# Optimization experiments

Hardware: AMD Instinct MI355X
Metric: run time of the kernel (lower is better)

## Reference

```python
import jax, jax.numpy as jnp
import numpy as np

TOP_K = 2

def setup_inputs() -> dict:
    key = jax.random.key(0)
    k1, k2, k3, k4, k5 = jax.random.split(key, 5)
    B, S, D, E, H = 1, 2048, 2048, 8, 5632
    scale = 0.02
    return {
        "x": jax.random.normal(k1, (B, S, D), dtype=jnp.float32),
        "gate_w": jax.random.normal(k2, (E, D), dtype=jnp.float32) * scale,
        "w1": jax.random.normal(k3, (E, H, D), dtype=jnp.float32) * scale,
        "w2": jax.random.normal(k4, (E, D, H), dtype=jnp.float32) * scale,
        "w3": jax.random.normal(k5, (E, H, D), dtype=jnp.float32) * scale,
    }


def reference(x, gate_w, w1, w2, w3):
    # x: [B, S, D]; gate_w: [E, D]; w1/w3: [E, H, D]; w2: [E, D, H]
    B, S, D = x.shape
    E = gate_w.shape[0]
    xf = x.reshape(-1, D)                      # [T, D]
    T = xf.shape[0]

    # Gate (gate_softmax=False): topk on raw scores, softmax over the top-k
    scores = xf @ gate_w.T                     # [T, E]
    expert_weights, expert_indices = jax.lax.top_k(scores, TOP_K)
    expert_weights = jax.nn.softmax(expert_weights, axis=-1)  # [T, K]

    # Scatter top-k weights to a dense [T, E] combine matrix (zeros elsewhere)
    combine = jnp.zeros((T, E), dtype=xf.dtype).at[
        jnp.arange(T)[:, None], expert_indices
    ].add(expert_weights)

    # SwiGLU FFN per expert, batched over the (small, fixed) expert axis.
    # Math identical to masked dispatch since combine is zero off the top-k.
    h = jax.nn.silu(jnp.einsum("td,ehd->eth", xf, w1)) \
        * jnp.einsum("td,ehd->eth", xf, w3)    # [E, T, H]
    ye = jnp.einsum("eth,edh->etd", h, w2)     # [E, T, D]

    # Weighted combine of top-k expert outputs per token
    y = jnp.einsum("etd,te->td", ye, combine)  # [T, D]
    return y.reshape(B, S, D)
```

## Files before the change

### kernel.cpp

```cpp
#include <hip/hip_runtime.h>
#include <hip/hip_bf16.h>

#define T_TOK 2048
#define DIM   2048
#define NE    8
#define NH    5632

typedef __attribute__((ext_vector_type(4))) float f32x4;
typedef __attribute__((ext_vector_type(8))) short short8;
typedef __attribute__((ext_vector_type(4))) unsigned int u32x4;
typedef __attribute__((ext_vector_type(4))) float float4v;

__device__ inline unsigned short f2bf(float f) {
    unsigned u = __builtin_bit_cast(unsigned, f);
    u += 0x7fffu + ((u >> 16) & 1u);
    return (unsigned short)(u >> 16);
}

__device__ __forceinline__ short8 pack8(float4v a, float4v b) {
    short8 o;
    o[0]=(short)f2bf(a[0]); o[1]=(short)f2bf(a[1]); o[2]=(short)f2bf(a[2]); o[3]=(short)f2bf(a[3]);
    o[4]=(short)f2bf(b[0]); o[5]=(short)f2bf(b[1]); o[6]=(short)f2bf(b[2]); o[7]=(short)f2bf(b[3]);
    return o;
}

__device__ __forceinline__ short8 cvt8(f32x4 lo, f32x4 hi) {
    u32x4 L = __builtin_bit_cast(u32x4, lo);
    u32x4 H = __builtin_bit_cast(u32x4, hi);
    u32x4 r;
    r[0] = __builtin_amdgcn_perm(L[1], L[0], 0x07060302u);
    r[1] = __builtin_amdgcn_perm(L[3], L[2], 0x07060302u);
    r[2] = __builtin_amdgcn_perm(H[1], H[0], 0x07060302u);
    r[3] = __builtin_amdgcn_perm(H[3], H[2], 0x07060302u);
    return __builtin_bit_cast(short8, r);
}

__device__ __forceinline__ void glds16(const void* g, void* l) {
    __builtin_amdgcn_global_load_lds((const __attribute__((address_space(1))) void*)g,
                                     (__attribute__((address_space(3))) void*)l, 16, 0, 0);
}

__global__ void k_cvt(const float* __restrict__ src, unsigned short* __restrict__ dst, int n8) {
    int i = blockIdx.x * blockDim.x + threadIdx.x;
    if (i >= n8) return;
    const float4v* xv = (const float4v*)src;
    ((short8*)dst)[i] = pack8(xv[2 * i], xv[2 * i + 1]);
}

__global__ void k_gate(const float* __restrict__ x, const float* __restrict__ gw,
                       int* __restrict__ rt_e, float* __restrict__ rt_w, int* __restrict__ cnt) {
    int wid = threadIdx.x >> 6, lane = threadIdx.x & 63;
    int t = blockIdx.x * 4 + wid;
    if (t >= T_TOK) return;
    float acc[NE];
#pragma unroll
    for (int e = 0; e < NE; e++) acc[e] = 0.f;
    const float* xr = x + (size_t)t * DIM;
    for (int d = lane; d < DIM; d += 64) {
        float xv = xr[d];
#pragma unroll
        for (int e = 0; e < NE; e++) acc[e] += xv * gw[e * DIM + d];
    }
#pragma unroll
    for (int e = 0; e < NE; e++) {
        float v = acc[e];
#pragma unroll
        for (int off = 32; off; off >>= 1) v += __shfl_xor(v, off);
        acc[e] = v;
    }
    if (lane == 0) {
        int i0 = 0; float s0 = acc[0];
#pragma unroll
        for (int e = 1; e < NE; e++) if (acc[e] > s0) { s0 = acc[e]; i0 = e; }
        int i1 = -1; float s1 = -1e30f;
#pragma unroll
        for (int e = 0; e < NE; e++) if (e != i0 && acc[e] > s1) { s1 = acc[e]; i1 = e; }
        float w0 = 1.f / (1.f + expf(s1 - s0));
        rt_e[2 * t] = i0; rt_e[2 * t + 1] = i1;
        rt_w[2 * t] = w0; rt_w[2 * t + 1] = 1.f - w0;
        atomicAdd(&cnt[i0], 1);
        atomicAdd(&cnt[i1], 1);
    }
}

__global__ void k_base(const int* __restrict__ cnt, int* __restrict__ base, int* __restrict__ pb) {
    if (threadIdx.x == 0) {
        int s = 0, p = 0;
        for (int e = 0; e < NE; e++) {
            base[e] = s; pb[e] = p;
            s += cnt[e];
            p += ((cnt[e] + 127) >> 7) << 7;
        }
    }
}

__global__ void k_assign(const int* __restrict__ rt_e, const float* __restrict__ rt_w,
                         const int* __restrict__ base, int* __restrict__ run,
                         int* __restrict__ tok, float* __restrict__ tw,
                         int* __restrict__ slotof) {
    int t = blockIdx.x * blockDim.x + threadIdx.x;
    if (t >= T_TOK) return;
#pragma unroll
    for (int k = 0; k < 2; k++) {
        int e = rt_e[2 * t + k];
        int p = atomicAdd(&run[e], 1);
        int g = base[e] + p;
        tok[g] = t;
        tw[g] = rt_w[2 * t + k];
        slotof[2 * t + k] = g;
    }
}

__global__ void k_xpack(const float* __restrict__ x,
                        const int* __restrict__ cnt, const int* __restrict__ base,
                        const int* __restrict__ pb, const int* __restrict__ tok,
                        unsigned short* __restrict__ xp) {
    int e = blockIdx.z, mt = blockIdx.y, kt = blockIdx.x;
    int c = cnt[e], m0 = mt * 128;
    if (m0 >= c) return;
    int gb = base[e];
    int ptile = (pb[e] >> 7) + mt;
    int lane = threadIdx.x & 63, w = threadIdx.x >> 6;
    int kc = lane & 7;
    unsigned short* db = xp + (size_t)ptile * 262144 + (size_t)kt * 8192;
#pragma unroll
    for (int it = 0; it < 4; ++it) {
        int rloc = it * 32 + w * 8 + (lane >> 3);
        int slot = m0 + rloc;
        int t = tok[gb + (slot < c ? slot : 0)];
        const float* s = x + (size_t)t * DIM + kt * 64 + kc * 8;
        *(short8*)(db + kc * 1024 + rloc * 8) = pack8(*(const float4v*)s, *(const float4v*)(s + 4));
    }
}

__global__ void k_combine(const float* __restrict__ ye, const int* __restrict__ slotof,
                          float* __restrict__ y) {
    int t = blockIdx.x;
    int s0 = slotof[2 * t], s1 = slotof[2 * t + 1];
    const float4v* a = (const float4v*)(ye + (size_t)s0 * DIM);
    const float4v* b = (const float4v*)(ye + (size_t)s1 * DIM);
    float4v* o = (float4v*)(y + (size_t)t * DIM);
    for (int i = threadIdx.x; i < DIM / 4; i += 256) {
        float4v va = a[i], vb = b[i];
        float4v r;
        r[0] = va[0] + vb[0]; r[1] = va[1] + vb[1];
        r[2] = va[2] + vb[2]; r[3] = va[3] + vb[3];
        o[i] = r;
    }
}

__launch_bounds__(256, 3)
__global__ void k_ffn1p(const unsigned short* __restrict__ xp,
                        const float* __restrict__ w1, const float* __restrict__ w3,
                        const int* __restrict__ cnt, const int* __restrict__ pb,
                        unsigned short* __restrict__ hb, int nwg,
                        const float* __restrict__ w2, unsigned short* __restrict__ w2p) {
    int bid = blockIdx.x;
    if (bid >= nwg) {
        int pid = bid - nwg;
        int kt = pid % 88;
        int r  = pid / 88;
        int nt = r & 15;
        int e  = r >> 4;
        int lane = threadIdx.x & 63, w = threadIdx.x >> 6;
        int kc = lane & 7;
        const float* sb = w2 + (size_t)e * DIM * NH;
        unsigned short* db = w2p + ((size_t)(e * 16 + nt) * 88 + kt) * 8192;
#pragma unroll
        for (int it = 0; it < 4; ++it) {
            int rloc = it * 32 + w * 8 + (lane >> 3);
            const float* s = sb + (size_t)(nt * 128 + rloc) * NH + kt * 64 + kc * 8;
            *(short8*)(db + kc * 1024 + rloc * 8) = pack8(*(const float4v*)s, *(const float4v*)(s + 4));
        }
        return;
    }

    int swz = (bid & 7) * (nwg >> 3) + (bid >> 3);
    int mt = swz & 15;
    int r2 = swz >> 4;
    int nt = r2 % 88;
    int e  = r2 / 88;
    int c  = cnt[e];
    int m0 = mt * 128;
    if (m0 >= c) return;
    int ptile = (pb[e] >> 7) + mt;

    __shared__ unsigned short As[8192];
    __shared__ float B1f[4096];
    __shared__ float B3f[4096];

    int tid = threadIdx.x;
    int lane = tid & 63, w = tid >> 6;
    int wm = w >> 1, wn = w & 1;
    int half = w & 1, wh = w >> 1;
    int p15 = lane & 15, rl0 = lane >> 4;

    const unsigned short* aB = xp + (size_t)ptile * 262144 + half * 512 + lane * 8;
    const float* w1e = w1 + (size_t)(e * NH + nt * 64) * DIM;
    const float* w3e = w3 + (size_t)(e * NH + nt * 64) * DIM;

    f32x4 acc1[4][2], acc3[4][2];
#pragma unroll
    for (int i = 0; i < 4; i++)
#pragma unroll
        for (int j = 0; j < 2; j++) { acc1[i][j] = (f32x4)0.f; acc3[i][j] = (f32x4)0.f; }

    for (int kt = 0; kt < 32; ++kt) {
        __syncthreads();
#pragma unroll
        for (int i = 0; i < 4; i++) {
            int kc = i * 2 + wh;
            glds16(aB + kt * 8192 + kc * 1024, (char*)As + kc * 2048 + half * 1024);
        }
#pragma unroll
        for (int i = 0; i < 4; i++) {
            int rloc = w * 16 + i * 4 + rl0;
            int q    = p15 ^ ((i * 4 + rl0) & 15);
            glds16(w1e + (size_t)rloc * DIM + kt * 64 + q * 4, (char*)B1f + (w * 16 + i * 4) * 256);
            glds16(w3e + (size_t)rloc * DIM + kt * 64 + q * 4, (char*)B3f + (w * 16 + i * 4) * 256);
        }
        asm volatile("s_waitcnt vmcnt(0)" ::: "memory");
        __syncthreads();
#pragma unroll
        for (int kh = 0; kh < 2; kh++) {
            int kc = kh * 4 + rl0;
            short8 a[4], b1[2], b3[2];
#pragma unroll
            for (int mf = 0; mf < 4; mf++) {
                int r = wm * 64 + mf * 16 + p15;
                a[mf] = *(const short8*)(As + kc * 1024 + r * 8);
            }
#pragma unroll
            for (int nf = 0; nf < 2; nf++) {
                int rb = wn * 32 + nf * 16 + p15;
                const float* rB1 = B1f + rb * 64;
                const float* rB3 = B3f + rb * 64;
                int o0 = ((2 * kc) ^ p15) << 2, o1 = ((2 * kc + 1) ^ p15) << 2;
                b1[nf] = cvt8(*(const f32x4*)(rB1 + o0), *(const f32x4*)(rB1 + o1));
                b3[nf] = cvt8(*(const f32x4*)(rB3 + o0), *(const f32x4*)(rB3 + o1));
            }
#pragma unroll
            for (int mf = 0; mf < 4; mf++)
#pragma unroll
                for (int nf = 0; nf < 2; nf++) {
                    acc1[mf][nf] = __builtin_amdgcn_mfma_f32_16x16x32_bf16(a[mf], b1[nf], acc1[mf][nf], 0, 0, 0);
                    acc3[mf][nf] = __builtin_amdgcn_mfma_f32_16x16x32_bf16(a[mf], b3[nf], acc3[mf][nf], 0, 0, 0);
                }
        }
    }

    unsigned short* hT = hb + ((size_t)ptile * 88 + nt) * 8192;
#pragma unroll
    for (int mf = 0; mf < 4; mf++)
#pragma unroll
        for (int nf = 0; nf < 2; nf++)
#pragma unroll
            for (int r = 0; r < 4; r++) {
                int row = wm * 64 + mf * 16 + (rl0 << 2) + r;
                int col = wn * 32 + nf * 16 + p15;
                if (m0 + row < c) {
                    float a = acc1[mf][nf][r];
                    float g = a / (1.f + expf(-a));
                    float v = g * acc3[mf][nf][r];
                    hT[(col >> 3) * 1024 + row * 8 + (col & 7)] = f2bf(v);
                }
            }
}

__launch_bounds__(256, 4)
__global__ void k_ffn2(const unsigned short* __restrict__ hb,
                       const unsigned short* __restrict__ w2p,
                       const int* __restrict__ cnt, const int* __restrict__ base,
                       const int* __restrict__ pb,
                       const float* __restrict__ tw,
                       float* __restrict__ ye, int nwg) {
    int bid = blockIdx.x;
    int swz = (bid & 7) * (nwg >> 3) + (bid >> 3);
    int mt = swz & 15;
    int r2 = swz >> 4;
    int nt = r2 & 15;
    int e  = r2 >> 4;
    int c  = cnt[e];
    int m0 = mt * 128;
    if (m0 >= c) return;
    int gb = base[e];
    int ptile = (pb[e] >> 7) + mt;
    int n0 = nt * 128;

    __shared__ unsigned short As[8192];
    __shared__ unsigned short Bs[8192];
    __shared__ float gws[128];

    int tid = threadIdx.x;
    if (tid < 128) {
        int s = m0 + tid;
        gws[tid] = (s < c) ? tw[gb + s] : 0.f;
    }

    int lane = tid & 63, w = tid >> 6;
    int wm = w >> 1, wn = w & 1;
    int half = w & 1, wh = w >> 1;

    const unsigned short* aB = hb  + (size_t)ptile * 720896 + half * 512 + lane * 8;
    const unsigned short* bB = w2p + (size_t)(e * 16 + nt) * 720896 + half * 512 + lane * 8;

    f32x4 acc[4][4];
#pragma unroll
    for (int i = 0; i < 4; i++)
#pragma unroll
        for (int j = 0; j < 4; j++) acc[i][j] = (f32x4)0.f;

    for (int kt = 0; kt < 88; ++kt) {
        __syncthreads();
#pragma unroll
        for (int i = 0; i < 4; i++) {
            int kc = i * 2 + wh;
            glds16(aB + kt * 8192 + kc * 1024, (char*)As + kc * 2048 + half * 1024);
            glds16(bB + kt * 8192 + kc * 1024, (char*)Bs + kc * 2048 + half * 1024);
        }
        asm volatile("s_waitcnt vmcnt(0)" ::: "memory");
        __syncthreads();
#pragma unroll
        for (int kh = 0; kh < 2; kh++) {
            int kc = kh * 4 + (lane >> 4);
            short8 a[4], b[4];
#pragma unroll
            for (int mf = 0; mf < 4; mf++) {
                int r = wm * 64 + mf * 16 + (lane & 15);
                a[mf] = *(const short8*)(As + kc * 1024 + r * 8);
            }
#pragma unroll
            for (int nf = 0; nf < 4; nf++) {
                int rb = wn * 64 + nf * 16 + (lane & 15);
                b[nf] = *(const short8*)(Bs + kc * 1024 + rb * 8);
            }
#pragma unroll
            for (int mf = 0; mf < 4; mf++)
#pragma unroll
                for (int nf = 0; nf < 4; nf++)
                    acc[mf][nf] = __builtin_amdgcn_mfma_f32_16x16x32_bf16(a[mf], b[nf], acc[mf][nf], 0, 0, 0);
        }
    }

#pragma unroll
    for (int mf = 0; mf < 4; mf++)
#pragma unroll
        for (int nf = 0; nf < 4; nf++)
#pragma unroll
            for (int r = 0; r < 4; r++) {
                int row = wm * 64 + mf * 16 + ((lane >> 4) << 2) + r;
                int col = wn * 64 + nf * 16 + (lane & 15);
                if (m0 + row < c) {
                    ye[(size_t)(gb + m0 + row) * DIM + n0 + col] = gws[row] * acc[mf][nf][r];
                }
            }
}

__launch_bounds__(256)
__global__ void k_ffn1_fb(const unsigned short* __restrict__ xb,
                          const float* __restrict__ w1, const float* __restrict__ w3,
                          const int* __restrict__ cnt, const int* __restrict__ base,
                          const int* __restrict__ tok, unsigned short* __restrict__ hbuf) {
    int e  = blockIdx.x >> 4;
    int mt = blockIdx.x & 15;
    int c  = cnt[e];
    int m0 = mt * 128;
    if (m0 >= c) return;
    int gb = base[e];
    int n0 = blockIdx.y * 64;

    __shared__ unsigned short As[128 * 64];
    __shared__ unsigned short B1s[64 * 64];
    __shared__ unsigned short B3s[64 * 64];
    __shared__ int toks[128];

    int tid = threadIdx.x;
    if (tid < 128) {
        int s = m0 + tid;
        toks[tid] = (s < c) ? tok[gb + s] : tok[gb];
    }
    int lane = tid & 63, wid = tid >> 6;
    int wm = wid >> 1, wn = wid & 1;

    f32x4 acc1[4][2], acc3[4][2];
#pragma unroll
    for (int i = 0; i < 4; i++)
#pragma unroll
        for (int j = 0; j < 2; j++) { acc1[i][j] = (f32x4)0.f; acc3[i][j] = (f32x4)0.f; }

    const float* W1 = w1 + (size_t)e * NH * DIM + (size_t)n0 * DIM;
    const float* W3 = w3 + (size_t)e * NH * DIM + (size_t)n0 * DIM;

    for (int kt = 0; kt < DIM / 64; ++kt) {
        int k0 = kt * 64;
        __syncthreads();
#pragma unroll
        for (int i = 0; i < 4; i++) {
            int f = i * 256 + tid;
            int row = f >> 3, ch = f & 7;
            u32x4 v = *(const u32x4*)(xb + (size_t)toks[row] * DIM + k0 + ch * 8);
            *(u32x4*)(As + row * 64 + ((ch ^ (row & 7)) << 3)) = v;
        }
#pragma unroll
        for (int i = 0; i < 2; i++) {
            int f = i * 256 + tid;
            int row = f >> 3, ch = f & 7;
            {
                const float* src = W1 + (size_t)row * DIM + k0 + ch * 8;
                *(short8*)(B1s + row * 64 + ((ch ^ (row & 7)) << 3)) =
                    pack8(*(const float4v*)src, *(const float4v*)(src + 4));
            }
            {
                const float* src = W3 + (size_t)row * DIM + k0 + ch * 8;
                *(short8*)(B3s + row * 64 + ((ch ^ (row & 7)) << 3)) =
                    pack8(*(const float4v*)src, *(const float4v*)(src + 4));
            }
        }
        __syncthreads();
#pragma unroll
        for (int kk = 0; kk < 2; kk++) {
            int kch = kk * 4 + (lane >> 4);
            short8 af[4], b1f[2], b3f[2];
#pragma unroll
            for (int mf = 0; mf < 4; mf++) {
                int r = wm * 64 + mf * 16 + (lane & 15);
                af[mf] = *(const short8*)(As + r * 64 + ((kch ^ (r & 7)) << 3));
            }
#pragma unroll
            for (int nf = 0; nf < 2; nf++) {
                int r = wn * 32 + nf * 16 + (lane & 15);
                b1f[nf] = *(const short8*)(B1s + r * 64 + ((kch ^ (r & 7)) << 3));
                b3f[nf] = *(const short8*)(B3s + r * 64 + ((kch ^ (r & 7)) << 3));
            }
#pragma unroll
            for (int mf = 0; mf < 4; mf++)
#pragma unroll
                for (int nf = 0; nf < 2; nf++) {
                    acc1[mf][nf] = __builtin_amdgcn_mfma_f32_16x16x32_bf16(af[mf], b1f[nf], acc1[mf][nf], 0, 0, 0);
                    acc3[mf][nf] = __builtin_amdgcn_mfma_f32_16x16x32_bf16(af[mf], b3f[nf], acc3[mf][nf], 0, 0, 0);
                }
        }
    }
#pragma unroll
    for (int mf = 0; mf < 4; mf++)
#pragma unroll
        for (int nf = 0; nf < 2; nf++)
#pragma unroll
            for (int r = 0; r < 4; r++) {
                int row = wm * 64 + mf * 16 + ((lane >> 4) << 2) + r;
                int col = wn * 32 + nf * 16 + (lane & 15);
                if (m0 + row < c) {
                    float a = acc1[mf][nf][r];
                    float g = a / (1.f + expf(-a));
                    float v = g * acc3[mf][nf][r];
                    hbuf[(size_t)(gb + m0 + row) * NH + n0 + col] = f2bf(v);
                }
            }
}

__launch_bounds__(256)
__global__ void k_ffn2_fb(const unsigned short* __restrict__ hbuf,
                          const float* __restrict__ w2,
                          const int* __restrict__ cnt, const int* __restrict__ base,
                          const int* __restrict__ tok, const float* __restrict__ tw,
                          float* __restrict__ y) {
    int e  = blockIdx.x >> 4;
    int mt = blockIdx.x & 15;
    int c  = cnt[e];
    int m0 = mt * 128;
    if (m0 >= c) return;
    int gb = base[e];
    int n0 = blockIdx.y * 128;

    __shared__ unsigned short As[128 * 64];
    __shared__ unsigned short Bs[128 * 64];
    __shared__ int   toks[128];
    __shared__ float gws[128];

    int tid = threadIdx.x;
    if (tid < 128) {
        int s = m0 + tid;
        toks[tid] = (s < c) ? tok[gb + s] : 0;
        gws[tid]  = (s < c) ? tw[gb + s] : 0.f;
    }
    int lane = tid & 63, wid = tid >> 6;
    int wm = wid >> 1, wn = wid & 1;

    f32x4 acc[4][4];
#pragma unroll
    for (int i = 0; i < 4; i++)
#pragma unroll
        for (int j = 0; j < 4; j++) acc[i][j] = (f32x4)0.f;

    const float* W2 = w2 + (size_t)e * DIM * NH + (size_t)n0 * NH;

    for (int kt = 0; kt < NH / 64; ++kt) {
        int k0 = kt * 64;
        __syncthreads();
#pragma unroll
        for (int i = 0; i < 4; i++) {
            int f = i * 256 + tid;
            int row = f >> 3, ch = f & 7;
            int rr = m0 + row; rr = (rr < c) ? rr : (c - 1);
            u32x4 v = *(const u32x4*)(hbuf + (size_t)(gb + rr) * NH + k0 + ch * 8);
            *(u32x4*)(As + row * 64 + ((ch ^ (row & 7)) << 3)) = v;
        }
#pragma unroll
        for (int i = 0; i < 4; i++) {
            int f = i * 256 + tid;
            int row = f >> 3, ch = f & 7;
            const float* src = W2 + (size_t)row * NH + k0 + ch * 8;
            *(short8*)(Bs + row * 64 + ((ch ^ (row & 7)) << 3)) =
                pack8(*(const float4v*)src, *(const float4v*)(src + 4));
        }
        __syncthreads();
#pragma unroll
        for (int kk = 0; kk < 2; kk++) {
            int kch = kk * 4 + (lane >> 4);
            short8 af[4], bf[4];
#pragma unroll
            for (int mf = 0; mf < 4; mf++) {
                int r = wm * 64 + mf * 16 + (lane & 15);
                af[mf] = *(const short8*)(As + r * 64 + ((kch ^ (r & 7)) << 3));
            }
#pragma unroll
            for (int nf = 0; nf < 4; nf++) {
                int r = wn * 64 + nf * 16 + (lane & 15);
                bf[nf] = *(const short8*)(Bs + r * 64 + ((kch ^ (r & 7)) << 3));
            }
#pragma unroll
            for (int mf = 0; mf < 4; mf++)
#pragma unroll
                for (int nf = 0; nf < 4; nf++)
                    acc[mf][nf] = __builtin_amdgcn_mfma_f32_16x16x32_bf16(af[mf], bf[nf], acc[mf][nf], 0, 0, 0);
        }
    }
#pragma unroll
    for (int mf = 0; mf < 4; mf++)
#pragma unroll
        for (int nf = 0; nf < 4; nf++)
#pragma unroll
            for (int r = 0; r < 4; r++) {
                int row = wm * 64 + mf * 16 + ((lane >> 4) << 2) + r;
                int col = wn * 64 + nf * 16 + (lane & 15);
                if (m0 + row < c) {
                    float v = gws[row] * acc[mf][nf][r];
                    atomicAdd(&y[(size_t)toks[row] * DIM + n0 + col], v);
                }
            }
}

extern "C" void kernel_launch(void* const* d_in, const int* in_sizes, int n_in,
                              void* d_out, int out_size, void* d_ws, size_t ws_size,
                              hipStream_t stream) {
    const float* x  = (const float*)d_in[0];
    const float* gw = (const float*)d_in[1];
    const float* w1 = (const float*)d_in[2];
    const float* w2 = (const float*)d_in[3];
    const float* w3 = (const float*)d_in[4];
    float* y = (float*)d_out;

    char* ws = (char*)d_ws;
    int*   cnt  = (int*)(ws + 0);
    int*   run  = (int*)(ws + 64);
    int*   basep= (int*)(ws + 128);
    int*   pb   = (int*)(ws + 192);
    int*   tok  = (int*)(ws + 256);
    float* tw   = (float*)(ws + 16640);
    int*   rt_e = (int*)(ws + 33024);
    float* rt_w = (float*)(ws + 49408);
    unsigned short* xp    = (unsigned short*)(ws + 66048);
    unsigned short* hbufp = (unsigned short*)(ws + 21037568);
    unsigned short* w2p   = (unsigned short*)(ws + 78709248);
    int*   slotof = (int*)(ws + 263258624);
    float* ye     = (float*)(ws + 263275008);
    const size_t needed = 296829440ull;

    hipMemsetAsync(ws, 0, 256, stream);

    if (ws_size >= needed) {
        k_gate<<<T_TOK / 4, 256, 0, stream>>>(x, gw, rt_e, rt_w, cnt);
        k_base<<<1, 64, 0, stream>>>(cnt, basep, pb);
        k_assign<<<T_TOK / 256, 256, 0, stream>>>(rt_e, rt_w, basep, run, tok, tw, slotof);
        k_xpack<<<dim3(32, 16, NE), 256, 0, stream>>>(x, cnt, basep, pb, tok, xp);
        int nwg1 = NE * 16 * 88;
        int nwg2 = NE * 16 * 16;
        k_ffn1p<<<nwg1 + 11264, 256, 0, stream>>>(xp, w1, w3, cnt, pb, hbufp, nwg1, w2, w2p);
        k_ffn2<<<nwg2, 256, 0, stream>>>(hbufp, w2p, cnt, basep, pb, tw, ye, nwg2);
        k_combine<<<T_TOK, 256, 0, stream>>>(ye, slotof, y);
    } else {
        hipMemsetAsync(d_out, 0, (size_t)out_size * sizeof(float), stream);
        k_gate<<<T_TOK / 4, 256, 0, stream>>>(x, gw, rt_e, rt_w, cnt);
        k_base<<<1, 64, 0, stream>>>(cnt, basep, pb);
        k_assign<<<T_TOK / 256, 256, 0, stream>>>(rt_e, rt_w, basep, run, tok, tw, (int*)(ws + 49408 + 16384));
        k_cvt<<<(T_TOK * DIM / 8) / 256, 256, 0, stream>>>(x, xp, T_TOK * DIM / 8);
        k_ffn1_fb<<<dim3(NE * 16, NH / 64), 256, 0, stream>>>(xp, w1, w3, cnt, basep, tok, hbufp);
        k_ffn2_fb<<<dim3(NE * 16, DIM / 128), 256, 0, stream>>>(hbufp, w2, cnt, basep, tok, tw, y);
    }
}
```

Baseline: 778.7 us.

## Halve ffn1 N-tile to 32 columns and raise occupancy to five waves

The gate/up GEMM kernel now computes 32 hidden columns per workgroup instead of 64. Shared-memory B buffers and accumulators are halved, the grid doubles, and launch bounds rise from 3 to 5 blocks per CU. The aim is more concurrent workgroups to hide global load latency. In exchange, each A tile is reloaded twice as often and each LDS load feeds fewer MFMAs.

```diff
diff --git a/kernel.cpp b/kernel.cpp
--- a/kernel.cpp
+++ b/kernel.cpp
@@ -149,7 +149,7 @@
     }
 }
 
-__launch_bounds__(256, 3)
+__launch_bounds__(256, 5)
 __global__ void k_ffn1p(const unsigned short* __restrict__ xp,
                         const float* __restrict__ w1, const float* __restrict__ w3,
                         const int* __restrict__ cnt, const int* __restrict__ pb,
@@ -160,16 +160,16 @@
         int pid = bid - nwg;
         int kt = pid % 88;
         int r  = pid / 88;
-        int nt = r & 15;
+        int nt2 = r & 15;
         int e  = r >> 4;
         int lane = threadIdx.x & 63, w = threadIdx.x >> 6;
         int kc = lane & 7;
         const float* sb = w2 + (size_t)e * DIM * NH;
-        unsigned short* db = w2p + ((size_t)(e * 16 + nt) * 88 + kt) * 8192;
+        unsigned short* db = w2p + ((size_t)(e * 16 + nt2) * 88 + kt) * 8192;
 #pragma unroll
         for (int it = 0; it < 4; ++it) {
             int rloc = it * 32 + w * 8 + (lane >> 3);
-            const float* s = sb + (size_t)(nt * 128 + rloc) * NH + kt * 64 + kc * 8;
+            const float* s = sb + (size_t)(nt2 * 128 + rloc) * NH + kt * 64 + kc * 8;
             *(short8*)(db + kc * 1024 + rloc * 8) = pack8(*(const float4v*)s, *(const float4v*)(s + 4));
         }
         return;
@@ -178,16 +178,16 @@
     int swz = (bid & 7) * (nwg >> 3) + (bid >> 3);
     int mt = swz & 15;
     int r2 = swz >> 4;
-    int nt = r2 % 88;
-    int e  = r2 / 88;
+    int nt = r2 % 176;
+    int e  = r2 / 176;
     int c  = cnt[e];
     int m0 = mt * 128;
     if (m0 >= c) return;
     int ptile = (pb[e] >> 7) + mt;
 
     __shared__ unsigned short As[8192];
-    __shared__ float B1f[4096];
-    __shared__ float B3f[4096];
+    __shared__ float B1f[2048];
+    __shared__ float B3f[2048];
 
     int tid = threadIdx.x;
     int lane = tid & 63, w = tid >> 6;
@@ -196,14 +196,12 @@
     int p15 = lane & 15, rl0 = lane >> 4;
 
     const unsigned short* aB = xp + (size_t)ptile * 262144 + half * 512 + lane * 8;
-    const float* w1e = w1 + (size_t)(e * NH + nt * 64) * DIM;
-    const float* w3e = w3 + (size_t)(e * NH + nt * 64) * DIM;
-
-    f32x4 acc1[4][2], acc3[4][2];
-#pragma unroll
-    for (int i = 0; i < 4; i++)
-#pragma unroll
-        for (int j = 0; j < 2; j++) { acc1[i][j] = (f32x4)0.f; acc3[i][j] = (f32x4)0.f; }
+    const float* w1e = w1 + (size_t)(e * NH + nt * 32) * DIM;
+    const float* w3e = w3 + (size_t)(e * NH + nt * 32) * DIM;
+
+    f32x4 acc1[4], acc3[4];
+#pragma unroll
+    for (int i = 0; i < 4; i++) { acc1[i] = (f32x4)0.f; acc3[i] = (f32x4)0.f; }
 
     for (int kt = 0; kt < 32; ++kt) {
         __syncthreads();
@@ -213,58 +211,53 @@
             glds16(aB + kt * 8192 + kc * 1024, (char*)As + kc * 2048 + half * 1024);
         }
 #pragma unroll
-        for (int i = 0; i < 4; i++) {
-            int rloc = w * 16 + i * 4 + rl0;
-            int q    = p15 ^ ((i * 4 + rl0) & 15);
-            glds16(w1e + (size_t)rloc * DIM + kt * 64 + q * 4, (char*)B1f + (w * 16 + i * 4) * 256);
-            glds16(w3e + (size_t)rloc * DIM + kt * 64 + q * 4, (char*)B3f + (w * 16 + i * 4) * 256);
+        for (int i = 0; i < 2; i++) {
+            int rloc = w * 8 + i * 4 + rl0;
+            int q    = p15 ^ (rloc & 15);
+            glds16(w1e + (size_t)rloc * DIM + kt * 64 + q * 4, (char*)B1f + (w * 8 + i * 4) * 256);
+            glds16(w3e + (size_t)rloc * DIM + kt * 64 + q * 4, (char*)B3f + (w * 8 + i * 4) * 256);
         }
         asm volatile("s_waitcnt vmcnt(0)" ::: "memory");
         __syncthreads();
 #pragma unroll
         for (int kh = 0; kh < 2; kh++) {
             int kc = kh * 4 + rl0;
-            short8 a[4], b1[2], b3[2];
+            short8 a[4], b1, b3;
 #pragma unroll
             for (int mf = 0; mf < 4; mf++) {
                 int r = wm * 64 + mf * 16 + p15;
                 a[mf] = *(const short8*)(As + kc * 1024 + r * 8);
             }
-#pragma unroll
-            for (int nf = 0; nf < 2; nf++) {
-                int rb = wn * 32 + nf * 16 + p15;
+            {
+                int rb = wn * 16 + p15;
                 const float* rB1 = B1f + rb * 64;
                 const float* rB3 = B3f + rb * 64;
                 int o0 = ((2 * kc) ^ p15) << 2, o1 = ((2 * kc + 1) ^ p15) << 2;
-                b1[nf] = cvt8(*(const f32x4*)(rB1 + o0), *(const f32x4*)(rB1 + o1));
-                b3[nf] = cvt8(*(const f32x4*)(rB3 + o0), *(const f32x4*)(rB3 + o1));
-            }
-#pragma unroll
-            for (int mf = 0; mf < 4; mf++)
-#pragma unroll
-                for (int nf = 0; nf < 2; nf++) {
-                    acc1[mf][nf] = __builtin_amdgcn_mfma_f32_16x16x32_bf16(a[mf], b1[nf], acc1[mf][nf], 0, 0, 0);
-                    acc3[mf][nf] = __builtin_amdgcn_mfma_f32_16x16x32_bf16(a[mf], b3[nf], acc3[mf][nf], 0, 0, 0);
-                }
-        }
-    }
-
-    unsigned short* hT = hb + ((size_t)ptile * 88 + nt) * 8192;
+                b1 = cvt8(*(const f32x4*)(rB1 + o0), *(const f32x4*)(rB1 + o1));
+                b3 = cvt8(*(const f32x4*)(rB3 + o0), *(const f32x4*)(rB3 + o1));
+            }
+#pragma unroll
+            for (int mf = 0; mf < 4; mf++) {
+                acc1[mf] = __builtin_amdgcn_mfma_f32_16x16x32_bf16(a[mf], b1, acc1[mf], 0, 0, 0);
+                acc3[mf] = __builtin_amdgcn_mfma_f32_16x16x32_bf16(a[mf], b3, acc3[mf], 0, 0, 0);
+            }
+        }
+    }
+
+    unsigned short* hT = hb + ((size_t)ptile * 88 + (nt >> 1)) * 8192;
+    int colbase = (nt & 1) * 32 + wn * 16 + p15;
 #pragma unroll
     for (int mf = 0; mf < 4; mf++)
 #pragma unroll
-        for (int nf = 0; nf < 2; nf++)
-#pragma unroll
-            for (int r = 0; r < 4; r++) {
-                int row = wm * 64 + mf * 16 + (rl0 << 2) + r;
-                int col = wn * 32 + nf * 16 + p15;
-                if (m0 + row < c) {
-                    float a = acc1[mf][nf][r];
-                    float g = a / (1.f + expf(-a));
-                    float v = g * acc3[mf][nf][r];
-                    hT[(col >> 3) * 1024 + row * 8 + (col & 7)] = f2bf(v);
-                }
-            }
+        for (int r = 0; r < 4; r++) {
+            int row = wm * 64 + mf * 16 + (rl0 << 2) + r;
+            if (m0 + row < c) {
+                float a = acc1[mf][r];
+                float g = a / (1.f + expf(-a));
+                float v = g * acc3[mf][r];
+                hT[(colbase >> 3) * 1024 + row * 8 + (colbase & 7)] = f2bf(v);
+            }
+        }
 }
 
 __launch_bounds__(256, 4)
@@ -583,7 +576,7 @@
         k_base<<<1, 64, 0, stream>>>(cnt, basep, pb);
         k_assign<<<T_TOK / 256, 256, 0, stream>>>(rt_e, rt_w, basep, run, tok, tw, slotof);
         k_xpack<<<dim3(32, 16, NE), 256, 0, stream>>>(x, cnt, basep, pb, tok, xp);
-        int nwg1 = NE * 16 * 88;
+        int nwg1 = NE * 16 * 176;
         int nwg2 = NE * 16 * 16;
         k_ffn1p<<<nwg1 + 11264, 256, 0, stream>>>(xp, w1, w3, cnt, pb, hbufp, nwg1, w2, w2p);
         k_ffn2<<<nwg2, 256, 0, stream>>>(hbufp, w2p, cnt, basep, pb, tw, ye, nwg2);
```

After: 846.0 us. 1.09x slower.
